# Performance work log

Measured on AMD Instinct MI355X. Metric: run time of the kernel, lower is better.

The kernel has to match this reference:

```python
import jax, jax.numpy as jnp
import numpy as np

N_EMBD = 1024
HEAD_SIZE = 64
BATCH = 4
T = 4096  # == block_size


def setup_inputs() -> dict:
    key = jax.random.key(0)
    kx, kq, kk, kv = jax.random.split(key, 4)
    x = jax.random.normal(kx, (BATCH, T, N_EMBD), dtype=jnp.float32)
    Wq = jax.random.normal(kq, (N_EMBD, HEAD_SIZE), dtype=jnp.float32) * 0.02
    Wk = jax.random.normal(kk, (N_EMBD, HEAD_SIZE), dtype=jnp.float32) * 0.02
    Wv = jax.random.normal(kv, (N_EMBD, HEAD_SIZE), dtype=jnp.float32) * 0.02
    return {"x": x, "Wq": Wq, "Wk": Wk, "Wv": Wv}


def reference(x, Wq, Wk, Wv):
    # x: [B, T, C]; projections: [B, T, H]
    B, Tlen, C = x.shape
    q = jnp.einsum('btc,ch->bth', x, Wq)
    k = jnp.einsum('btc,ch->bth', x, Wk)
    v = jnp.einsum('btc,ch->bth', x, Wv)
    # NOTE: original scales by C**-0.5 where C = n_embd (input channels), not head_size
    scale = jnp.asarray(C, x.dtype) ** -0.5
    wei = jnp.einsum('bth,bsh->bts', q, k) * scale  # [B, T, T]
    causal = jnp.tril(jnp.ones((Tlen, Tlen), dtype=bool))
    wei = jnp.where(causal, wei, -jnp.inf)
    wei = jax.nn.softmax(wei, axis=-1)
    # dropout p=0.0 -> identity
    out = jnp.einsum('bts,bsh->bth', wei, v)  # [B, T, H]
    return out
```

## Files before the change

### kernel.cpp

```cpp
#include <hip/hip_runtime.h>
#include <math.h>

#define T_SEQ 4096
#define NBATCH 4
#define NEMBD 1024
#define HS 64
#define BT (NBATCH * T_SEQ)

typedef float f32x4 __attribute__((ext_vector_type(4)));
typedef short s8v  __attribute__((ext_vector_type(8)));
typedef short s4v  __attribute__((ext_vector_type(4)));

__device__ __forceinline__ short f2b(float f) {
    union { float f; unsigned u; } v; v.f = f;
    unsigned r = v.u + 0x7fffu + ((v.u >> 16) & 1u);
    return (short)(r >> 16);
}

__global__ __launch_bounds__(256) void wtrans_kernel(
        const float* __restrict__ Wq, const float* __restrict__ Wk,
        const float* __restrict__ Wv, short* __restrict__ Wt) {
    int e = blockIdx.x * 256 + threadIdx.x;
    int col = e & 63;
    int k   = (e >> 6) & 1023;
    int mat = e >> 16;
    const float* W = (mat == 0) ? Wq : ((mat == 1) ? Wk : Wv);
    Wt[(size_t)(mat * 64 + col) * 1024 + k] = f2b(W[k * 64 + col]);
}

__global__ __launch_bounds__(256) void proj_kernel(
        const float* __restrict__ x, const short* __restrict__ Wt,
        short* __restrict__ QKV) {
    __shared__ short xt[32 * 72];
    int tid = threadIdx.x;
    int w = tid >> 6, l = tid & 63, quad = l >> 4, c16 = l & 15;
    int row0 = blockIdx.x * 32;
    short* VpT = QKV + 2 * (size_t)BT * HS;

    f32x4 acc[2][3] = {};
    for (int ko = 0; ko < NEMBD; ko += 64) {
        {
            int r = tid >> 3, kc = (tid & 7) * 8;
            const float* gx = x + (size_t)(row0 + r) * NEMBD + ko + kc;
            float4 a = *(const float4*)gx;
            float4 b = *(const float4*)(gx + 4);
            s8v v;
            v[0]=f2b(a.x); v[1]=f2b(a.y); v[2]=f2b(a.z); v[3]=f2b(a.w);
            v[4]=f2b(b.x); v[5]=f2b(b.y); v[6]=f2b(b.z); v[7]=f2b(b.w);
            *(s8v*)(xt + r * 72 + kc) = v;
        }
        __syncthreads();
        #pragma unroll
        for (int kk = 0; kk < 64; kk += 32) {
            s8v af[2], bf[3];
            #pragma unroll
            for (int i = 0; i < 2; i++)
                af[i] = *(const s8v*)(xt + (i * 16 + c16) * 72 + kk + quad * 8);
            #pragma unroll
            for (int j = 0; j < 3; j++)
                bf[j] = *(const s8v*)(Wt + (size_t)(w * 48 + j * 16 + c16) * 1024 + ko + kk + quad * 8);
            #pragma unroll
            for (int i = 0; i < 2; i++)
                #pragma unroll
                for (int j = 0; j < 3; j++)
                    acc[i][j] = __builtin_amdgcn_mfma_f32_16x16x32_bf16(af[i], bf[j], acc[i][j], 0, 0, 0);
        }
        __syncthreads();
    }
    #pragma unroll
    for (int i = 0; i < 2; i++)
        #pragma unroll
        for (int j = 0; j < 3; j++) {
            int g = w * 48 + j * 16 + c16;
            int mat = g >> 6, h = g & 63;
            if (mat < 2) {
                #pragma unroll
                for (int r = 0; r < 4; r++) {
                    int row = row0 + i * 16 + quad * 4 + r;
                    QKV[(size_t)mat * BT * HS + (size_t)row * HS + h] = f2b(acc[i][j][r]);
                }
            } else {
                s4v pv;
                #pragma unroll
                for (int r = 0; r < 4; r++) pv[r] = f2b(acc[i][j][r]);
                *(s4v*)(VpT + (size_t)h * BT + row0 + i * 16 + quad * 4) = pv;
            }
        }
}

__global__ __launch_bounds__(256) void attn_kernel(
        const short* __restrict__ QKV, float* __restrict__ out) {
    __shared__ float fbuf[5120];
    short* Pb = (short*)fbuf;

    int tid = threadIdx.x;
    int w = tid >> 6, l = tid & 63, quad = l >> 4, c16 = l & 15;
    int bi = blockIdx.x;
    int b  = bi & 3;
    int jr = bi >> 2;
    int jt = (jr < 128) ? (255 - jr) : (jr - 128);
    int q0 = jt * 16;

    const short* Qp  = QKV;
    const short* Kp  = QKV + (size_t)BT * HS;
    const short* VpT = QKV + 2 * (size_t)BT * HS;
    size_t bT = (size_t)b * T_SEQ;

    s8v qf0 = *(const s8v*)(Qp + (bT + q0 + c16) * HS + quad * 8);
    s8v qf1 = *(const s8v*)(Qp + (bT + q0 + c16) * HS + quad * 8 + 32);

    f32x4 o[4] = {};
    float lsum[4] = {0.f, 0.f, 0.f, 0.f};
    const float cs = 0.03125f * 1.44269504088896f;
    int nkt = (q0 >> 6) + 1;
    short* Pw = Pb + w * (16 * 72);

    for (int kt = w; kt < nkt; kt += 4) {
        int kb = kt * 64;
        f32x4 s[4];
        #pragma unroll
        for (int nt = 0; nt < 4; nt++) {
            const short* kr = Kp + (bT + kb + nt * 16 + c16) * HS;
            s8v bk0 = *(const s8v*)(kr + quad * 8);
            s8v bk1 = *(const s8v*)(kr + quad * 8 + 32);
            f32x4 z = {0.f, 0.f, 0.f, 0.f};
            z = __builtin_amdgcn_mfma_f32_16x16x32_bf16(qf0, bk0, z, 0, 0, 0);
            z = __builtin_amdgcn_mfma_f32_16x16x32_bf16(qf1, bk1, z, 0, 0, 0);
            s[nt] = z;
        }
        bool last = (kt == nkt - 1);
        #pragma unroll
        for (int nt = 0; nt < 4; nt++)
            #pragma unroll
            for (int r = 0; r < 4; r++) {
                float v = s[nt][r] * cs;
                if (last && (kb + nt * 16 + c16 > q0 + quad * 4 + r)) v = -30000.f;
                float p = exp2f(v);
                s[nt][r] = p;
                lsum[r] += p;
            }
        #pragma unroll
        for (int nt = 0; nt < 4; nt++)
            #pragma unroll
            for (int r = 0; r < 4; r++)
                Pw[(quad * 4 + r) * 72 + nt * 16 + c16] = f2b(s[nt][r]);
        s8v pa0 = *(const s8v*)(Pw + c16 * 72 + quad * 8);
        s8v pa1 = *(const s8v*)(Pw + c16 * 72 + quad * 8 + 32);
        #pragma unroll
        for (int nt = 0; nt < 4; nt++) {
            const short* vr = VpT + (size_t)(nt * 16 + c16) * BT + bT + kb;
            s8v bv0 = *(const s8v*)(vr + quad * 8);
            s8v bv1 = *(const s8v*)(vr + quad * 8 + 32);
            o[nt] = __builtin_amdgcn_mfma_f32_16x16x32_bf16(pa0, bv0, o[nt], 0, 0, 0);
            o[nt] = __builtin_amdgcn_mfma_f32_16x16x32_bf16(pa1, bv1, o[nt], 0, 0, 0);
        }
    }

    #pragma unroll
    for (int r = 0; r < 4; r++)
        #pragma unroll
        for (int off = 8; off >= 1; off >>= 1)
            lsum[r] += __shfl_xor(lsum[r], off);

    __syncthreads();
    float* slot = fbuf + (w * 64 + l) * 20;
    #pragma unroll
    for (int nt = 0; nt < 4; nt++) *(f32x4*)(slot + nt * 4) = o[nt];
    #pragma unroll
    for (int r = 0; r < 4; r++) slot[16 + r] = lsum[r];
    __syncthreads();
    if (w == 0) {
        f32x4 oo[4] = {};
        float ll[4] = {0.f, 0.f, 0.f, 0.f};
        #pragma unroll
        for (int g = 0; g < 4; g++) {
            const float* sp = fbuf + (g * 64 + l) * 20;
            #pragma unroll
            for (int nt = 0; nt < 4; nt++) oo[nt] += *(const f32x4*)(sp + nt * 4);
            #pragma unroll
            for (int r = 0; r < 4; r++) ll[r] += sp[16 + r];
        }
        #pragma unroll
        for (int nt = 0; nt < 4; nt++)
            #pragma unroll
            for (int r = 0; r < 4; r++)
                out[(bT + q0 + quad * 4 + r) * HS + nt * 16 + c16] = oo[nt][r] / ll[r];
    }
}

extern "C" void kernel_launch(void* const* d_in, const int* in_sizes, int n_in,
                              void* d_out, int out_size, void* d_ws, size_t ws_size,
                              hipStream_t stream) {
    const float* x  = (const float*)d_in[0];
    const float* Wq = (const float*)d_in[1];
    const float* Wk = (const float*)d_in[2];
    const float* Wv = (const float*)d_in[3];
    float* out = (float*)d_out;

    short* QKV = (short*)d_ws;
    short* Wt  = QKV + (size_t)3 * BT * HS;

    wtrans_kernel<<<768, 256, 0, stream>>>(Wq, Wk, Wv, Wt);
    proj_kernel<<<BT / 32, 256, 0, stream>>>(x, Wt, QKV);
    attn_kernel<<<1024, 256, 0, stream>>>(QKV, out);
}
```

Before: 181.4 us.

## Restructure attention to 32-row query tiles with 8 waves and fold scale into Wq

The attention kernel now gives each block a 32-query tile and 8 waves. Each K and V fragment loaded is reused across two 16-row query sub-tiles, and S is computed transposed so P can be packed with perm instructions. The softmax scale and log2e are folded into Wq during the weight transpose, and x is converted to bf16 by truncation, packed straight into MFMA operands with no LDS staging or barriers. The cross-wave reduction is reworked for 8 waves, and the grid is halved with a 512-thread block. The trade-offs are truncating instead of round-to-nearest for x and P, higher register pressure, and coarser causal load balance since the previous pairing of long and short tiles is dropped.

```diff
diff --git a/kernel.cpp b/kernel.cpp
--- a/kernel.cpp
+++ b/kernel.cpp
@@ -11,64 +11,59 @@
 typedef short s8v  __attribute__((ext_vector_type(8)));
 typedef short s4v  __attribute__((ext_vector_type(4)));
 
-__device__ __forceinline__ short f2b(float f) {
+__device__ __forceinline__ short f2b_rne(float f) {
     union { float f; unsigned u; } v; v.f = f;
     unsigned r = v.u + 0x7fffu + ((v.u >> 16) & 1u);
     return (short)(r >> 16);
+}
+__device__ __forceinline__ unsigned pk2(float lo, float hi) {
+    return __builtin_amdgcn_perm(__float_as_uint(hi), __float_as_uint(lo), 0x07060302u);
 }
 
 __global__ __launch_bounds__(256) void wtrans_kernel(
         const float* __restrict__ Wq, const float* __restrict__ Wk,
         const float* __restrict__ Wv, short* __restrict__ Wt) {
     int e = blockIdx.x * 256 + threadIdx.x;
-    int col = e & 63;
-    int k   = (e >> 6) & 1023;
-    int mat = e >> 16;
+    int col = e & 63, k = (e >> 6) & 1023, mat = e >> 16;
     const float* W = (mat == 0) ? Wq : ((mat == 1) ? Wk : Wv);
-    Wt[(size_t)(mat * 64 + col) * 1024 + k] = f2b(W[k * 64 + col]);
+    float scale = (mat == 0) ? 0.0450842298f : 1.0f;
+    Wt[(size_t)(mat * 64 + col) * 1024 + k] = f2b_rne(W[k * 64 + col] * scale);
 }
 
 __global__ __launch_bounds__(256) void proj_kernel(
         const float* __restrict__ x, const short* __restrict__ Wt,
         short* __restrict__ QKV) {
-    __shared__ short xt[32 * 72];
     int tid = threadIdx.x;
     int w = tid >> 6, l = tid & 63, quad = l >> 4, c16 = l & 15;
     int row0 = blockIdx.x * 32;
     short* VpT = QKV + 2 * (size_t)BT * HS;
 
+    const float* xr0 = x + (size_t)(row0 + c16) * NEMBD;
+    const float* xr1 = x + (size_t)(row0 + 16 + c16) * NEMBD;
+    const short* wp  = Wt + (size_t)(w * 48 + c16) * 1024;
+
     f32x4 acc[2][3] = {};
-    for (int ko = 0; ko < NEMBD; ko += 64) {
-        {
-            int r = tid >> 3, kc = (tid & 7) * 8;
-            const float* gx = x + (size_t)(row0 + r) * NEMBD + ko + kc;
-            float4 a = *(const float4*)gx;
-            float4 b = *(const float4*)(gx + 4);
-            s8v v;
-            v[0]=f2b(a.x); v[1]=f2b(a.y); v[2]=f2b(a.z); v[3]=f2b(a.w);
-            v[4]=f2b(b.x); v[5]=f2b(b.y); v[6]=f2b(b.z); v[7]=f2b(b.w);
-            *(s8v*)(xt + r * 72 + kc) = v;
-        }
-        __syncthreads();
-        #pragma unroll
-        for (int kk = 0; kk < 64; kk += 32) {
-            s8v af[2], bf[3];
-            #pragma unroll
-            for (int i = 0; i < 2; i++)
-                af[i] = *(const s8v*)(xt + (i * 16 + c16) * 72 + kk + quad * 8);
-            #pragma unroll
-            for (int j = 0; j < 3; j++)
-                bf[j] = *(const s8v*)(Wt + (size_t)(w * 48 + j * 16 + c16) * 1024 + ko + kk + quad * 8);
-            #pragma unroll
-            for (int i = 0; i < 2; i++)
-                #pragma unroll
-                for (int j = 0; j < 3; j++)
-                    acc[i][j] = __builtin_amdgcn_mfma_f32_16x16x32_bf16(af[i], bf[j], acc[i][j], 0, 0, 0);
-        }
-        __syncthreads();
-    }
-    #pragma unroll
-    for (int i = 0; i < 2; i++)
+    for (int ko = 0; ko < NEMBD; ko += 32) {
+        int off = ko + quad * 8;
+        union { s8v v; unsigned u[4]; } a0, a1;
+        float4 p0 = *(const float4*)(xr0 + off), p1 = *(const float4*)(xr0 + off + 4);
+        a0.u[0] = pk2(p0.x, p0.y); a0.u[1] = pk2(p0.z, p0.w);
+        a0.u[2] = pk2(p1.x, p1.y); a0.u[3] = pk2(p1.z, p1.w);
+        float4 r0 = *(const float4*)(xr1 + off), r1 = *(const float4*)(xr1 + off + 4);
+        a1.u[0] = pk2(r0.x, r0.y); a1.u[1] = pk2(r0.z, r0.w);
+        a1.u[2] = pk2(r1.x, r1.y); a1.u[3] = pk2(r1.z, r1.w);
+        s8v b0 = *(const s8v*)(wp + off);
+        s8v b1 = *(const s8v*)(wp + 16 * 1024 + off);
+        s8v b2 = *(const s8v*)(wp + 32 * 1024 + off);
+        acc[0][0] = __builtin_amdgcn_mfma_f32_16x16x32_bf16(a0.v, b0, acc[0][0], 0, 0, 0);
+        acc[0][1] = __builtin_amdgcn_mfma_f32_16x16x32_bf16(a0.v, b1, acc[0][1], 0, 0, 0);
+        acc[0][2] = __builtin_amdgcn_mfma_f32_16x16x32_bf16(a0.v, b2, acc[0][2], 0, 0, 0);
+        acc[1][0] = __builtin_amdgcn_mfma_f32_16x16x32_bf16(a1.v, b0, acc[1][0], 0, 0, 0);
+        acc[1][1] = __builtin_amdgcn_mfma_f32_16x16x32_bf16(a1.v, b1, acc[1][1], 0, 0, 0);
+        acc[1][2] = __builtin_amdgcn_mfma_f32_16x16x32_bf16(a1.v, b2, acc[1][2], 0, 0, 0);
+    }
+    #pragma unroll
+    for (int rg = 0; rg < 2; rg++)
         #pragma unroll
         for (int j = 0; j < 3; j++) {
             int g = w * 48 + j * 16 + c16;
@@ -76,115 +71,125 @@
             if (mat < 2) {
                 #pragma unroll
                 for (int r = 0; r < 4; r++) {
-                    int row = row0 + i * 16 + quad * 4 + r;
-                    QKV[(size_t)mat * BT * HS + (size_t)row * HS + h] = f2b(acc[i][j][r]);
+                    int row = row0 + rg * 16 + quad * 4 + r;
+                    QKV[(size_t)mat * BT * HS + (size_t)row * HS + h] = f2b_rne(acc[rg][j][r]);
                 }
             } else {
                 s4v pv;
                 #pragma unroll
-                for (int r = 0; r < 4; r++) pv[r] = f2b(acc[i][j][r]);
-                *(s4v*)(VpT + (size_t)h * BT + row0 + i * 16 + quad * 4) = pv;
-            }
-        }
-}
-
-__global__ __launch_bounds__(256) void attn_kernel(
+                for (int r = 0; r < 4; r++) pv[r] = f2b_rne(acc[rg][j][r]);
+                *(s4v*)(VpT + (size_t)h * BT + row0 + rg * 16 + quad * 4) = pv;
+            }
+        }
+}
+
+__global__ __launch_bounds__(512, 4) void attn_kernel(
         const short* __restrict__ QKV, float* __restrict__ out) {
-    __shared__ float fbuf[5120];
-    short* Pb = (short*)fbuf;
+    __shared__ float smem[9216];
+    short* Ps = (short*)smem;
 
     int tid = threadIdx.x;
     int w = tid >> 6, l = tid & 63, quad = l >> 4, c16 = l & 15;
     int bi = blockIdx.x;
     int b  = bi & 3;
-    int jr = bi >> 2;
-    int jt = (jr < 128) ? (255 - jr) : (jr - 128);
-    int q0 = jt * 16;
+    int jt = 127 - (bi >> 2);
+    int q0 = jt * 32;
 
     const short* Qp  = QKV;
     const short* Kp  = QKV + (size_t)BT * HS;
     const short* VpT = QKV + 2 * (size_t)BT * HS;
     size_t bT = (size_t)b * T_SEQ;
 
-    s8v qf0 = *(const s8v*)(Qp + (bT + q0 + c16) * HS + quad * 8);
-    s8v qf1 = *(const s8v*)(Qp + (bT + q0 + c16) * HS + quad * 8 + 32);
-
-    f32x4 o[4] = {};
-    float lsum[4] = {0.f, 0.f, 0.f, 0.f};
-    const float cs = 0.03125f * 1.44269504088896f;
+    s8v qf[2][2];
+    #pragma unroll
+    for (int qt = 0; qt < 2; qt++)
+        #pragma unroll
+        for (int h = 0; h < 2; h++)
+            qf[qt][h] = *(const s8v*)(Qp + (bT + q0 + qt * 16 + c16) * HS + h * 32 + quad * 8);
+
+    f32x4 o[2][4] = {};
+    float lsum[2] = {0.f, 0.f};
     int nkt = (q0 >> 6) + 1;
-    short* Pw = Pb + w * (16 * 72);
-
-    for (int kt = w; kt < nkt; kt += 4) {
+    short* Pw[2] = { Ps + (w * 2) * 1152, Ps + (w * 2 + 1) * 1152 };
+
+    for (int kt = w; kt < nkt; kt += 8) {
         int kb = kt * 64;
-        f32x4 s[4];
+        bool last = (kt == nkt - 1);
+        f32x4 st[2][4];
         #pragma unroll
         for (int nt = 0; nt < 4; nt++) {
-            const short* kr = Kp + (bT + kb + nt * 16 + c16) * HS;
-            s8v bk0 = *(const s8v*)(kr + quad * 8);
-            s8v bk1 = *(const s8v*)(kr + quad * 8 + 32);
-            f32x4 z = {0.f, 0.f, 0.f, 0.f};
-            z = __builtin_amdgcn_mfma_f32_16x16x32_bf16(qf0, bk0, z, 0, 0, 0);
-            z = __builtin_amdgcn_mfma_f32_16x16x32_bf16(qf1, bk1, z, 0, 0, 0);
-            s[nt] = z;
-        }
-        bool last = (kt == nkt - 1);
+            const short* kr = Kp + (bT + kb + nt * 16 + c16) * HS + quad * 8;
+            s8v k0 = *(const s8v*)kr;
+            s8v k1 = *(const s8v*)(kr + 32);
+            f32x4 z0 = {0.f, 0.f, 0.f, 0.f}, z1 = {0.f, 0.f, 0.f, 0.f};
+            z0 = __builtin_amdgcn_mfma_f32_16x16x32_bf16(k0, qf[0][0], z0, 0, 0, 0);
+            z0 = __builtin_amdgcn_mfma_f32_16x16x32_bf16(k1, qf[0][1], z0, 0, 0, 0);
+            z1 = __builtin_amdgcn_mfma_f32_16x16x32_bf16(k0, qf[1][0], z1, 0, 0, 0);
+            z1 = __builtin_amdgcn_mfma_f32_16x16x32_bf16(k1, qf[1][1], z1, 0, 0, 0);
+            st[0][nt] = z0; st[1][nt] = z1;
+        }
+        #pragma unroll
+        for (int qt = 0; qt < 2; qt++) {
+            int qrow = q0 + qt * 16 + c16;
+            #pragma unroll
+            for (int nt = 0; nt < 4; nt++) {
+                float p[4];
+                #pragma unroll
+                for (int r = 0; r < 4; r++) {
+                    float v = st[qt][nt][r];
+                    if (last && (kb + nt * 16 + quad * 4 + r > qrow)) v = -30000.f;
+                    p[r] = __builtin_amdgcn_exp2f(v);
+                    lsum[qt] += p[r];
+                }
+                union { s4v v; unsigned u[2]; } pkv;
+                pkv.u[0] = pk2(p[0], p[1]); pkv.u[1] = pk2(p[2], p[3]);
+                *(s4v*)(Pw[qt] + c16 * 72 + nt * 16 + quad * 4) = pkv.v;
+            }
+        }
+        s8v pa[2][2];
+        #pragma unroll
+        for (int qt = 0; qt < 2; qt++) {
+            pa[qt][0] = *(const s8v*)(Pw[qt] + c16 * 72 + quad * 8);
+            pa[qt][1] = *(const s8v*)(Pw[qt] + c16 * 72 + quad * 8 + 32);
+        }
+        #pragma unroll
+        for (int nt = 0; nt < 4; nt++) {
+            const short* vr = VpT + (size_t)(nt * 16 + c16) * BT + bT + kb + quad * 8;
+            s8v v0 = *(const s8v*)vr;
+            s8v v1 = *(const s8v*)(vr + 32);
+            #pragma unroll
+            for (int qt = 0; qt < 2; qt++) {
+                o[qt][nt] = __builtin_amdgcn_mfma_f32_16x16x32_bf16(pa[qt][0], v0, o[qt][nt], 0, 0, 0);
+                o[qt][nt] = __builtin_amdgcn_mfma_f32_16x16x32_bf16(pa[qt][1], v1, o[qt][nt], 0, 0, 0);
+            }
+        }
+    }
+
+    #pragma unroll
+    for (int qt = 0; qt < 2; qt++) {
+        lsum[qt] += __shfl_xor(lsum[qt], 16);
+        lsum[qt] += __shfl_xor(lsum[qt], 32);
+    }
+
+    #pragma unroll
+    for (int qt = 0; qt < 2; qt++) {
+        __syncthreads();
         #pragma unroll
         for (int nt = 0; nt < 4; nt++)
-            #pragma unroll
-            for (int r = 0; r < 4; r++) {
-                float v = s[nt][r] * cs;
-                if (last && (kb + nt * 16 + c16 > q0 + quad * 4 + r)) v = -30000.f;
-                float p = exp2f(v);
-                s[nt][r] = p;
-                lsum[r] += p;
-            }
-        #pragma unroll
-        for (int nt = 0; nt < 4; nt++)
+            *(f32x4*)(smem + ((w * 4 + nt) * 64 + l) * 4) = o[qt][nt];
+        if (l < 16) smem[8192 + w * 16 + l] = lsum[qt];
+        __syncthreads();
+        if (w < 4) {
+            f32x4 os = {0.f, 0.f, 0.f, 0.f}, ls = {0.f, 0.f, 0.f, 0.f};
+            #pragma unroll
+            for (int s = 0; s < 8; s++) {
+                os += *(const f32x4*)(smem + ((s * 4 + w) * 64 + l) * 4);
+                ls += *(const f32x4*)(smem + 8192 + s * 16 + quad * 4);
+            }
             #pragma unroll
             for (int r = 0; r < 4; r++)
-                Pw[(quad * 4 + r) * 72 + nt * 16 + c16] = f2b(s[nt][r]);
-        s8v pa0 = *(const s8v*)(Pw + c16 * 72 + quad * 8);
-        s8v pa1 = *(const s8v*)(Pw + c16 * 72 + quad * 8 + 32);
-        #pragma unroll
-        for (int nt = 0; nt < 4; nt++) {
-            const short* vr = VpT + (size_t)(nt * 16 + c16) * BT + bT + kb;
-            s8v bv0 = *(const s8v*)(vr + quad * 8);
-            s8v bv1 = *(const s8v*)(vr + quad * 8 + 32);
-            o[nt] = __builtin_amdgcn_mfma_f32_16x16x32_bf16(pa0, bv0, o[nt], 0, 0, 0);
-            o[nt] = __builtin_amdgcn_mfma_f32_16x16x32_bf16(pa1, bv1, o[nt], 0, 0, 0);
-        }
-    }
-
-    #pragma unroll
-    for (int r = 0; r < 4; r++)
-        #pragma unroll
-        for (int off = 8; off >= 1; off >>= 1)
-            lsum[r] += __shfl_xor(lsum[r], off);
-
-    __syncthreads();
-    float* slot = fbuf + (w * 64 + l) * 20;
-    #pragma unroll
-    for (int nt = 0; nt < 4; nt++) *(f32x4*)(slot + nt * 4) = o[nt];
-    #pragma unroll
-    for (int r = 0; r < 4; r++) slot[16 + r] = lsum[r];
-    __syncthreads();
-    if (w == 0) {
-        f32x4 oo[4] = {};
-        float ll[4] = {0.f, 0.f, 0.f, 0.f};
-        #pragma unroll
-        for (int g = 0; g < 4; g++) {
-            const float* sp = fbuf + (g * 64 + l) * 20;
-            #pragma unroll
-            for (int nt = 0; nt < 4; nt++) oo[nt] += *(const f32x4*)(sp + nt * 4);
-            #pragma unroll
-            for (int r = 0; r < 4; r++) ll[r] += sp[16 + r];
-        }
-        #pragma unroll
-        for (int nt = 0; nt < 4; nt++)
-            #pragma unroll
-            for (int r = 0; r < 4; r++)
-                out[(bT + q0 + quad * 4 + r) * HS + nt * 16 + c16] = oo[nt][r] / ll[r];
+                out[(bT + q0 + qt * 16 + quad * 4 + r) * HS + w * 16 + c16] = os[r] / ls[r];
+        }
     }
 }
 
@@ -202,5 +207,5 @@
 
     wtrans_kernel<<<768, 256, 0, stream>>>(Wq, Wk, Wv, Wt);
     proj_kernel<<<BT / 32, 256, 0, stream>>>(x, Wt, QKV);
-    attn_kernel<<<1024, 256, 0, stream>>>(QKV, out);
-}
+    attn_kernel<<<512, 512, 0, stream>>>(QKV, out);
+}
```

Measured after the change: 187.4 us. 1.03x slower.
